# Performance work log

Measured on AMD Instinct MI355X. Metric: run time of the kernel, lower is better.

Reference implementation:

```python
import jax, jax.numpy as jnp
import numpy as np

D = 768
HEAD_SIZE = 64  # D / num_heads = 768 / 12

def setup_inputs() -> dict:
    key = jax.random.key(0)
    k1, k2, k3, k4 = jax.random.split(key, 4)
    ix = jax.random.normal(k1, (8, 4096, D), dtype=jnp.float32)
    # Linear(D, head_size, bias=False) weights; stored as [D, head_size] for x @ W
    scale = 1.0 / np.sqrt(D)
    Wk = jax.random.uniform(k2, (D, HEAD_SIZE), dtype=jnp.float32, minval=-scale, maxval=scale)
    Wq = jax.random.uniform(k3, (D, HEAD_SIZE), dtype=jnp.float32, minval=-scale, maxval=scale)
    Wv = jax.random.uniform(k4, (D, HEAD_SIZE), dtype=jnp.float32, minval=-scale, maxval=scale)
    return {"ix": ix, "Wk": Wk, "Wq": Wq, "Wv": Wv}

def reference(ix, Wk, Wq, Wv):
    # ix: [B, S, D]
    k = ix @ Wk  # [B, S, H]
    q = ix @ Wq  # [B, S, H]
    v = ix @ Wv  # [B, S, H]
    scale = 1.0 / jnp.sqrt(jnp.asarray(HEAD_SIZE, ix.dtype))
    wei = jnp.einsum('bsh,bth->bst', q, k) * scale  # [B, S, S]
    wei = jax.nn.softmax(wei, axis=-1)
    out = jnp.einsum('bst,bth->bsh', wei, v)  # [B, S, H]
    return out
```

## Files before the change

kernel.cpp:

```cpp
#include <hip/hip_runtime.h>
#include <hip/hip_bf16.h>

#define D_DIM 768
#define HS 64
#define SEQ 4096
#define NBATCH 8

typedef short bf8 __attribute__((ext_vector_type(8)));
typedef short bf4v __attribute__((ext_vector_type(4)));
typedef float f4 __attribute__((ext_vector_type(4)));

static __device__ __forceinline__ short f2b(float x) {
    __hip_bfloat16 h = __float2bfloat16(x);
    return __builtin_bit_cast(short, h);
}

#if defined(__has_builtin)
#if __has_builtin(__builtin_amdgcn_exp2f)
#define EXP2F(x) __builtin_amdgcn_exp2f(x)
#endif
#endif
#ifndef EXP2F
#define EXP2F(x) exp2f(x)
#endif

__global__ __launch_bounds__(256) void wconv_kernel(
    const float* __restrict__ Wk, const float* __restrict__ Wq,
    const float* __restrict__ Wv, short* __restrict__ wt)
{
    int tid = blockIdx.x * 256 + threadIdx.x;
    int mat = tid / (D_DIM * HS);
    int rem = tid - mat * (D_DIM * HS);
    int k = rem >> 6;
    int n = rem & 63;
    const float* W = (mat == 0) ? Wk : (mat == 1) ? Wq : Wv;
    float scale = (mat == 1) ? 0.18033688011112042f : 1.0f;
    wt[(mat * HS + n) * D_DIM + k] = f2b(W[rem] * scale);
}

__global__ __launch_bounds__(256) void proj_kernel(
    const float* __restrict__ ix, const short* __restrict__ wt,
    short* __restrict__ qg, short* __restrict__ kg, short* __restrict__ vg)
{
    __shared__ short ixl[2][64 * 40];
    __shared__ short wtl[2][192 * 40];

    const int t = threadIdx.x;
    const int wave = t >> 6, lane = t & 63;
    const int m = lane & 15, quad = lane >> 4;
    const int wy = wave >> 1, wx = wave & 1;
    const int m0 = blockIdx.x * 64;

    const int srow = t >> 2;
    const int skoff = (t & 3) * 8;

    f4 xr0, xr1;
    bf8 wr0, wr1, wr2, wr3;

    auto load_chunk = [&](int c) {
        const float* px = ix + (m0 + srow) * D_DIM + c * 32 + skoff;
        xr0 = *(const f4*)px;
        xr1 = *(const f4*)(px + 4);
        if (t < 192) {
            const short* pw = wt + t * D_DIM + c * 32;
            wr0 = *(const bf8*)(pw);
            wr1 = *(const bf8*)(pw + 8);
            wr2 = *(const bf8*)(pw + 16);
            wr3 = *(const bf8*)(pw + 24);
        }
    };
    auto write_chunk = [&](int p) {
        bf8 xw;
        #pragma unroll
        for (int i = 0; i < 4; ++i) { xw[i] = f2b(xr0[i]); xw[i + 4] = f2b(xr1[i]); }
        *(bf8*)(&ixl[p][srow * 40 + skoff]) = xw;
        if (t < 192) {
            *(bf8*)(&wtl[p][t * 40 + 0])  = wr0;
            *(bf8*)(&wtl[p][t * 40 + 8])  = wr1;
            *(bf8*)(&wtl[p][t * 40 + 16]) = wr2;
            *(bf8*)(&wtl[p][t * 40 + 24]) = wr3;
        }
    };

    f4 acc[2][6] = {};

    load_chunk(0); write_chunk(0); __syncthreads();

    for (int c = 0; c < 24; ++c) {
        const int p = c & 1;
        if (c + 1 < 24) load_chunk(c + 1);

        bf8 a0 = *(const bf8*)(&ixl[p][(wy * 32 + m) * 40 + quad * 8]);
        bf8 a1 = *(const bf8*)(&ixl[p][(wy * 32 + 16 + m) * 40 + quad * 8]);
        bf8 bb[6];
        #pragma unroll
        for (int nt = 0; nt < 6; ++nt)
            bb[nt] = *(const bf8*)(&wtl[p][(wx * 96 + nt * 16 + m) * 40 + quad * 8]);
        #pragma unroll
        for (int nt = 0; nt < 6; ++nt) {
            acc[0][nt] = __builtin_amdgcn_mfma_f32_16x16x32_bf16(a0, bb[nt], acc[0][nt], 0, 0, 0);
            acc[1][nt] = __builtin_amdgcn_mfma_f32_16x16x32_bf16(a1, bb[nt], acc[1][nt], 0, 0, 0);
        }

        if (c + 1 < 24) { write_chunk((c + 1) & 1); __syncthreads(); }
    }

    #pragma unroll
    for (int mt = 0; mt < 2; ++mt) {
        const int row = m0 + wy * 32 + mt * 16 + quad * 4;
        #pragma unroll
        for (int nt = 0; nt < 6; ++nt) {
            const int cb = wx * 96 + nt * 16;
            short* op = (cb < 64) ? kg : (cb < 128) ? qg : vg;
            const int n = (cb & 63) + m;
            #pragma unroll
            for (int r = 0; r < 4; ++r)
                op[(row + r) * HS + n] = f2b(acc[mt][nt][r]);
        }
    }
}

__global__ __launch_bounds__(256) void attn_kernel(
    const short* __restrict__ qg, const short* __restrict__ kg,
    const short* __restrict__ vg, float* __restrict__ out)
{
    __shared__ short kl[2][64 * 72];
    __shared__ short vl[2][64 * 72];

    const int t = threadIdx.x;
    const int wave = t >> 6, lane = t & 63;
    const int m = lane & 15, quad = lane >> 4;
    const int b = blockIdx.y;
    const int rbase = b * SEQ;
    const int qw = blockIdx.x * 128 + wave * 32;

    bf8 qf[2][2];
    #pragma unroll
    for (int nq = 0; nq < 2; ++nq)
        #pragma unroll
        for (int st = 0; st < 2; ++st)
            qf[nq][st] = *(const bf8*)(qg + (rbase + qw + nq * 16 + m) * HS + st * 32 + quad * 8);

    const int srow = t >> 2;
    const int soff = (t & 3) * 16;

    uint4 kr0, kr1, vr0, vr1;
    auto load_chunk = [&](int c) {
        const short* pk = kg + (rbase + c * 64 + srow) * HS + soff;
        kr0 = *(const uint4*)pk; kr1 = *(const uint4*)(pk + 8);
        const short* pv = vg + (rbase + c * 64 + srow) * HS + soff;
        vr0 = *(const uint4*)pv; vr1 = *(const uint4*)(pv + 8);
    };
    auto write_chunk = [&](int p) {
        *(bf8*)(&kl[p][srow * 72 + soff])     = __builtin_bit_cast(bf8, kr0);
        *(bf8*)(&kl[p][srow * 72 + soff + 8]) = __builtin_bit_cast(bf8, kr1);
        bf8 v0 = __builtin_bit_cast(bf8, vr0), v1 = __builtin_bit_cast(bf8, vr1);
        #pragma unroll
        for (int i = 0; i < 8; ++i) {
            vl[p][(soff + i) * 72 + srow]     = v0[i];
            vl[p][(soff + 8 + i) * 72 + srow] = v1[i];
        }
    };

    f4 o[2][4] = {};
    float den[2] = {0.f, 0.f};

    load_chunk(0); write_chunk(0); __syncthreads();

    for (int c = 0; c < SEQ / 64; ++c) {
        const int p = c & 1;
        if (c + 1 < SEQ / 64) load_chunk(c + 1);

        #pragma unroll
        for (int kt = 0; kt < 4; ++kt) {
            bf8 ka0 = *(const bf8*)(&kl[p][(kt * 16 + m) * 72 + quad * 8]);
            bf8 ka1 = *(const bf8*)(&kl[p][(kt * 16 + m) * 72 + 32 + quad * 8]);
            bf4v vf[4];
            #pragma unroll
            for (int dt = 0; dt < 4; ++dt)
                vf[dt] = *(const bf4v*)(&vl[p][(dt * 16 + m) * 72 + kt * 16 + quad * 4]);
            #pragma unroll
            for (int nq = 0; nq < 2; ++nq) {
                f4 s = {0.f, 0.f, 0.f, 0.f};
                s = __builtin_amdgcn_mfma_f32_16x16x32_bf16(ka0, qf[nq][0], s, 0, 0, 0);
                s = __builtin_amdgcn_mfma_f32_16x16x32_bf16(ka1, qf[nq][1], s, 0, 0, 0);
                float e0 = EXP2F(s[0]);
                float e1 = EXP2F(s[1]);
                float e2 = EXP2F(s[2]);
                float e3 = EXP2F(s[3]);
                den[nq] += (e0 + e1) + (e2 + e3);
                bf4v pf;
                pf[0] = f2b(e0); pf[1] = f2b(e1); pf[2] = f2b(e2); pf[3] = f2b(e3);
                #pragma unroll
                for (int dt = 0; dt < 4; ++dt)
                    o[nq][dt] = __builtin_amdgcn_mfma_f32_16x16x16bf16_1k(vf[dt], pf, o[nq][dt], 0, 0, 0);
            }
        }

        if (c + 1 < SEQ / 64) { write_chunk((c + 1) & 1); __syncthreads(); }
    }

    #pragma unroll
    for (int nq = 0; nq < 2; ++nq) {
        float d = den[nq];
        d += __shfl_xor(d, 16, 64);
        d += __shfl_xor(d, 32, 64);
        const float r = 1.0f / d;
        const int orow = rbase + qw + nq * 16 + m;
        #pragma unroll
        for (int dt = 0; dt < 4; ++dt) {
            f4 res;
            #pragma unroll
            for (int i = 0; i < 4; ++i) res[i] = o[nq][dt][i] * r;
            *(f4*)(out + orow * HS + dt * 16 + quad * 4) = res;
        }
    }
}

extern "C" void kernel_launch(void* const* d_in, const int* in_sizes, int n_in,
                              void* d_out, int out_size, void* d_ws, size_t ws_size,
                              hipStream_t stream) {
    const float* ix = (const float*)d_in[0];
    const float* Wk = (const float*)d_in[1];
    const float* Wq = (const float*)d_in[2];
    const float* Wv = (const float*)d_in[3];
    float* out = (float*)d_out;

    short* qg = (short*)d_ws;
    short* kg = qg + (size_t)NBATCH * SEQ * HS;
    short* vg = kg + (size_t)NBATCH * SEQ * HS;
    short* wt = vg + (size_t)NBATCH * SEQ * HS;

    wconv_kernel<<<(3 * D_DIM * HS) / 256, 256, 0, stream>>>(Wk, Wq, Wv, wt);
    proj_kernel<<<(NBATCH * SEQ) / 64, 256, 0, stream>>>(ix, wt, qg, kg, vg);
    attn_kernel<<<dim3(SEQ / 128, NBATCH), 256, 0, stream>>>(qg, kg, vg, out);
}
```

Baseline: 257.6 us.

## Split attention over key halves, use 16x16x32 PV MFMA, add reduce kernel

The attention grid becomes 512 blocks, each handling half of the key sequence, so twice as many workgroups fill the CUs. It writes unnormalized numerators and denominators, and a new reduce kernel combines and normalizes them. The PV product now uses the 16x16x32 bf16 MFMA over 32 keys, with a repacked V transpose (row stride 70, paired 32-bit stores) and a cheaper round-half bf16 conversion. A block-index swizzle remaps batch and query tiles. In exchange it adds an extra kernel launch and fp32 partial-result traffic through the workspace.

```diff
diff --git a/kernel.cpp b/kernel.cpp
--- a/kernel.cpp
+++ b/kernel.cpp
@@ -7,12 +7,15 @@
 #define NBATCH 8
 
 typedef short bf8 __attribute__((ext_vector_type(8)));
-typedef short bf4v __attribute__((ext_vector_type(4)));
 typedef float f4 __attribute__((ext_vector_type(4)));
 
 static __device__ __forceinline__ short f2b(float x) {
     __hip_bfloat16 h = __float2bfloat16(x);
     return __builtin_bit_cast(short, h);
+}
+static __device__ __forceinline__ short f2b_rh(float x) {
+    unsigned u = __builtin_bit_cast(unsigned, x);
+    return (short)((u + 0x8000u) >> 16);
 }
 
 #if defined(__has_builtin)
@@ -122,17 +125,30 @@
 
 __global__ __launch_bounds__(256) void attn_kernel(
     const short* __restrict__ qg, const short* __restrict__ kg,
-    const short* __restrict__ vg, float* __restrict__ out)
+    const short* __restrict__ vg, float* __restrict__ num0,
+    float* __restrict__ num1, float* __restrict__ den0,
+    float* __restrict__ den1)
 {
     __shared__ short kl[2][64 * 72];
-    __shared__ short vl[2][64 * 72];
+    __shared__ short vl[2][64 * 70];
 
     const int t = threadIdx.x;
     const int wave = t >> 6, lane = t & 63;
     const int m = lane & 15, quad = lane >> 4;
-    const int b = blockIdx.y;
+
+    const int flat = blockIdx.x;
+    const int lg = (flat & 7) * 64 + (flat >> 3);
+    const int qx = lg & 31;
+    const int yz = lg >> 5;
+    const int ks = yz & 1;
+    const int b  = yz >> 1;
+
     const int rbase = b * SEQ;
-    const int qw = blockIdx.x * 128 + wave * 32;
+    const int kbase = rbase + ks * (SEQ / 2);
+    const int qw = qx * 128 + wave * 32;
+
+    float* __restrict__ nump = ks == 0 ? num0 : num1;
+    float* __restrict__ denp = ks == 0 ? den0 : den1;
 
     bf8 qf[2][2];
     #pragma unroll
@@ -141,15 +157,16 @@
         for (int st = 0; st < 2; ++st)
             qf[nq][st] = *(const bf8*)(qg + (rbase + qw + nq * 16 + m) * HS + st * 32 + quad * 8);
 
-    const int srow = t >> 2;
-    const int soff = (t & 3) * 16;
+    const int srow = t >> 2, soff = (t & 3) * 16;
+    const int jp = t >> 3, dg = t & 7;
+    const int j0 = jp * 2;
 
     uint4 kr0, kr1, vr0, vr1;
     auto load_chunk = [&](int c) {
-        const short* pk = kg + (rbase + c * 64 + srow) * HS + soff;
+        const short* pk = kg + (kbase + c * 64 + srow) * HS + soff;
         kr0 = *(const uint4*)pk; kr1 = *(const uint4*)(pk + 8);
-        const short* pv = vg + (rbase + c * 64 + srow) * HS + soff;
-        vr0 = *(const uint4*)pv; vr1 = *(const uint4*)(pv + 8);
+        const short* pv = vg + (kbase + c * 64 + j0) * HS + dg * 8;
+        vr0 = *(const uint4*)pv; vr1 = *(const uint4*)(pv + HS);
     };
     auto write_chunk = [&](int p) {
         *(bf8*)(&kl[p][srow * 72 + soff])     = __builtin_bit_cast(bf8, kr0);
@@ -157,8 +174,9 @@
         bf8 v0 = __builtin_bit_cast(bf8, vr0), v1 = __builtin_bit_cast(bf8, vr1);
         #pragma unroll
         for (int i = 0; i < 8; ++i) {
-            vl[p][(soff + i) * 72 + srow]     = v0[i];
-            vl[p][(soff + 8 + i) * 72 + srow] = v1[i];
+            const int d = dg * 8 + i;
+            unsigned val = (unsigned short)v0[i] | ((unsigned)(unsigned short)v1[i] << 16);
+            *(unsigned*)(&vl[p][d * 70 + j0]) = val;
         }
     };
 
@@ -167,37 +185,49 @@
 
     load_chunk(0); write_chunk(0); __syncthreads();
 
-    for (int c = 0; c < SEQ / 64; ++c) {
+    for (int c = 0; c < SEQ / 128; ++c) {
         const int p = c & 1;
-        if (c + 1 < SEQ / 64) load_chunk(c + 1);
-
-        #pragma unroll
-        for (int kt = 0; kt < 4; ++kt) {
-            bf8 ka0 = *(const bf8*)(&kl[p][(kt * 16 + m) * 72 + quad * 8]);
-            bf8 ka1 = *(const bf8*)(&kl[p][(kt * 16 + m) * 72 + 32 + quad * 8]);
-            bf4v vf[4];
+        if (c + 1 < SEQ / 128) load_chunk(c + 1);
+
+        #pragma unroll
+        for (int g = 0; g < 2; ++g) {
+            bf8 kA0 = *(const bf8*)(&kl[p][(g * 32 + m) * 72 + quad * 8]);
+            bf8 kA1 = *(const bf8*)(&kl[p][(g * 32 + m) * 72 + 32 + quad * 8]);
+            bf8 kB0 = *(const bf8*)(&kl[p][(g * 32 + 16 + m) * 72 + quad * 8]);
+            bf8 kB1 = *(const bf8*)(&kl[p][(g * 32 + 16 + m) * 72 + 32 + quad * 8]);
+
+            bf8 vf[4];
             #pragma unroll
-            for (int dt = 0; dt < 4; ++dt)
-                vf[dt] = *(const bf4v*)(&vl[p][(dt * 16 + m) * 72 + kt * 16 + quad * 4]);
+            for (int dt = 0; dt < 4; ++dt) {
+                const short* vp = &vl[p][(dt * 16 + m) * 70 + g * 32 + quad * 4];
+                unsigned a0 = *(const unsigned*)vp;
+                unsigned a1 = *(const unsigned*)(vp + 2);
+                unsigned b0 = *(const unsigned*)(vp + 16);
+                unsigned b1 = *(const unsigned*)(vp + 18);
+                uint4 u; u.x = a0; u.y = a1; u.z = b0; u.w = b1;
+                vf[dt] = __builtin_bit_cast(bf8, u);
+            }
+
             #pragma unroll
             for (int nq = 0; nq < 2; ++nq) {
-                f4 s = {0.f, 0.f, 0.f, 0.f};
-                s = __builtin_amdgcn_mfma_f32_16x16x32_bf16(ka0, qf[nq][0], s, 0, 0, 0);
-                s = __builtin_amdgcn_mfma_f32_16x16x32_bf16(ka1, qf[nq][1], s, 0, 0, 0);
-                float e0 = EXP2F(s[0]);
-                float e1 = EXP2F(s[1]);
-                float e2 = EXP2F(s[2]);
-                float e3 = EXP2F(s[3]);
-                den[nq] += (e0 + e1) + (e2 + e3);
-                bf4v pf;
-                pf[0] = f2b(e0); pf[1] = f2b(e1); pf[2] = f2b(e2); pf[3] = f2b(e3);
+                f4 sa = {0.f, 0.f, 0.f, 0.f}, sb = {0.f, 0.f, 0.f, 0.f};
+                sa = __builtin_amdgcn_mfma_f32_16x16x32_bf16(kA0, qf[nq][0], sa, 0, 0, 0);
+                sa = __builtin_amdgcn_mfma_f32_16x16x32_bf16(kA1, qf[nq][1], sa, 0, 0, 0);
+                sb = __builtin_amdgcn_mfma_f32_16x16x32_bf16(kB0, qf[nq][0], sb, 0, 0, 0);
+                sb = __builtin_amdgcn_mfma_f32_16x16x32_bf16(kB1, qf[nq][1], sb, 0, 0, 0);
+                float e0 = EXP2F(sa[0]), e1 = EXP2F(sa[1]), e2 = EXP2F(sa[2]), e3 = EXP2F(sa[3]);
+                float e4 = EXP2F(sb[0]), e5 = EXP2F(sb[1]), e6 = EXP2F(sb[2]), e7 = EXP2F(sb[3]);
+                den[nq] += ((e0 + e1) + (e2 + e3)) + ((e4 + e5) + (e6 + e7));
+                bf8 pf;
+                pf[0] = f2b_rh(e0); pf[1] = f2b_rh(e1); pf[2] = f2b_rh(e2); pf[3] = f2b_rh(e3);
+                pf[4] = f2b_rh(e4); pf[5] = f2b_rh(e5); pf[6] = f2b_rh(e6); pf[7] = f2b_rh(e7);
                 #pragma unroll
                 for (int dt = 0; dt < 4; ++dt)
-                    o[nq][dt] = __builtin_amdgcn_mfma_f32_16x16x16bf16_1k(vf[dt], pf, o[nq][dt], 0, 0, 0);
+                    o[nq][dt] = __builtin_amdgcn_mfma_f32_16x16x32_bf16(vf[dt], pf, o[nq][dt], 0, 0, 0);
             }
         }
 
-        if (c + 1 < SEQ / 64) { write_chunk((c + 1) & 1); __syncthreads(); }
+        if (c + 1 < SEQ / 128) { write_chunk((c + 1) & 1); __syncthreads(); }
     }
 
     #pragma unroll
@@ -205,16 +235,28 @@
         float d = den[nq];
         d += __shfl_xor(d, 16, 64);
         d += __shfl_xor(d, 32, 64);
-        const float r = 1.0f / d;
         const int orow = rbase + qw + nq * 16 + m;
-        #pragma unroll
-        for (int dt = 0; dt < 4; ++dt) {
-            f4 res;
-            #pragma unroll
-            for (int i = 0; i < 4; ++i) res[i] = o[nq][dt][i] * r;
-            *(f4*)(out + orow * HS + dt * 16 + quad * 4) = res;
-        }
-    }
+        if (quad == 0) denp[orow] = d;
+        #pragma unroll
+        for (int dt = 0; dt < 4; ++dt)
+            *(f4*)(nump + orow * HS + dt * 16 + quad * 4) = o[nq][dt];
+    }
+}
+
+__global__ __launch_bounds__(256) void reduce_kernel(
+    float* __restrict__ out, const float* __restrict__ num1,
+    const float* __restrict__ den0, const float* __restrict__ den1)
+{
+    const int gid = blockIdx.x * 256 + threadIdx.x;
+    const int base = gid * 4;
+    const int r = base >> 6;
+    f4 n0 = *(const f4*)(out + base);
+    f4 n1 = *(const f4*)(num1 + base);
+    const float rs = 1.0f / (den0[r] + den1[r]);
+    f4 res;
+    #pragma unroll
+    for (int i = 0; i < 4; ++i) res[i] = (n0[i] + n1[i]) * rs;
+    *(f4*)(out + base) = res;
 }
 
 extern "C" void kernel_launch(void* const* d_in, const int* in_sizes, int n_in,
@@ -226,12 +268,18 @@
     const float* Wv = (const float*)d_in[3];
     float* out = (float*)d_out;
 
+    const size_t NQKV = (size_t)NBATCH * SEQ * HS;
     short* qg = (short*)d_ws;
-    short* kg = qg + (size_t)NBATCH * SEQ * HS;
-    short* vg = kg + (size_t)NBATCH * SEQ * HS;
-    short* wt = vg + (size_t)NBATCH * SEQ * HS;
+    short* kg = qg + NQKV;
+    short* vg = kg + NQKV;
+    short* wt = vg + NQKV;
+    char*  fbase = (char*)(wt + 3 * D_DIM * HS);
+    float* num1 = (float*)fbase;
+    float* den0 = num1 + NQKV;
+    float* den1 = den0 + (size_t)NBATCH * SEQ;
 
     wconv_kernel<<<(3 * D_DIM * HS) / 256, 256, 0, stream>>>(Wk, Wq, Wv, wt);
     proj_kernel<<<(NBATCH * SEQ) / 64, 256, 0, stream>>>(ix, wt, qg, kg, vg);
-    attn_kernel<<<dim3(SEQ / 128, NBATCH), 256, 0, stream>>>(qg, kg, vg, out);
-}
+    attn_kernel<<<512, 256, 0, stream>>>(qg, kg, vg, out, num1, den0, den1);
+    reduce_kernel<<<(int)(NQKV / (256 * 4)), 256, 0, stream>>>(out, num1, den0, den1);
+}
```

New measurement: 228.2 us. 11.4% less time.
